# Optimization experiments

Measured on AMD Instinct MI355X. Metric: run time of the kernel, lower is better.

Reference implementation:

```python
import jax, jax.numpy as jnp
import numpy as np

B, S, DIM, NH = 2, 2048, 1024, 8
DH = DIM // NH
GATE_SOFT_CAP = 15.0
BACKEND_EPS = 5e-05
NORM_EPS = 1e-06


def setup_inputs() -> dict:
    key = jax.random.key(0)
    kq, kk, kv, kw = jax.random.split(key, 4)
    q = jax.random.normal(kq, (B, S, DIM), dtype=jnp.float32)
    k = jax.random.normal(kk, (B, S, DIM), dtype=jnp.float32)
    v = jax.random.normal(kv, (B, S, DIM), dtype=jnp.float32)
    # ifgate: Linear(3*dim, 2*num_heads). Init weight is zeros in the module;
    # use small random weights so the gate path is non-trivial.
    ifgate_w = 0.02 * jax.random.normal(kw, (2 * NH, 3 * DIM), dtype=jnp.float32)
    # bias per reset_parameters: i_bias = -10, f_bias = linspace(3, 6, NH)
    ifgate_b = jnp.concatenate([
        jnp.full((NH,), -10.0, dtype=jnp.float32),
        jnp.linspace(3.0, 6.0, NH, dtype=jnp.float32),
    ])
    # residual-weight RMSNorm gain: effective gain = 1 + outnorm_w (init zeros)
    outnorm_w = jnp.zeros((DIM,), dtype=jnp.float32)
    return {"q": q, "k": k, "v": v, "ifgate_w": ifgate_w,
            "ifgate_b": ifgate_b, "outnorm_w": outnorm_w}


def _mlstm_parallel(q, k, v, i_pre, f_pre):
    # q,k,v: (B,NH,S,DH); i_pre,f_pre: (B,NH,S). Native stabilized parallel mLSTM.
    log_fg = jax.nn.log_sigmoid(f_pre)                       # (B,NH,S)
    lf_cs = jnp.cumsum(log_fg, axis=-1)                      # (B,NH,S)
    lf = jnp.concatenate([jnp.zeros_like(lf_cs[..., :1]), lf_cs], axis=-1)  # (B,NH,S+1)
    # log_D[t, s] = sum_{j=s+1}^{t} log_fg[j] + i_pre[s]  for s <= t, else -inf
    log_d = lf[..., 1:, None] - lf[..., None, 1:] + i_pre[..., None, :]     # (B,NH,S,S)
    t_idx = jnp.arange(q.shape[2])
    mask = t_idx[:, None] >= t_idx[None, :]
    log_d = jnp.where(mask, log_d, -jnp.inf)
    m = jnp.max(log_d, axis=-1, keepdims=True)               # (B,NH,S,1)
    d_mat = jnp.exp(log_d - m)                               # stabilized decays
    scores = jnp.einsum("bhtd,bhsd->bhts", q, k) * (1.0 / np.sqrt(DH))
    s_mat = scores * d_mat                                   # (B,NH,S,S)
    denom = jnp.maximum(jnp.abs(jnp.sum(s_mat, axis=-1, keepdims=True)),
                        jnp.exp(-m)) + BACKEND_EPS
    return jnp.einsum("bhts,bhsd->bhtd", s_mat, v) / denom   # (B,NH,S,DH)


def reference(q, k, v, ifgate_w, ifgate_b, outnorm_w):
    b, s, dim = q.shape
    # gate preactivations from concatenated q,k,v with tanh soft cap
    gate_in = jnp.concatenate([q, k, v], axis=-1)            # (B,S,3*DIM)
    pre = gate_in @ ifgate_w.T + ifgate_b                    # (B,S,2*NH)
    pre = GATE_SOFT_CAP * jnp.tanh(pre / GATE_SOFT_CAP)
    i_pre = pre[..., :NH].transpose(0, 2, 1)                 # (B,NH,S)
    f_pre = pre[..., NH:].transpose(0, 2, 1)                 # (B,NH,S)
    # split heads
    qh = q.reshape(b, s, NH, DH).transpose(0, 2, 1, 3)
    kh = k.reshape(b, s, NH, DH).transpose(0, 2, 1, 3)
    vh = v.reshape(b, s, NH, DH).transpose(0, 2, 1, 3)
    h = _mlstm_parallel(qh, kh, vh, i_pre, f_pre)            # (B,NH,S,DH)
    # multi-head RMSNorm with residual gain (bias is unused in the module's forward)
    rrms = jax.lax.rsqrt(jnp.mean(h * h, axis=-1, keepdims=True) + NORM_EPS)
    gain = (1.0 + outnorm_w).reshape(1, NH, 1, DH)
    h = h * rrms * gain
    return h.transpose(0, 2, 1, 3).reshape(b, s, dim)
```

## Files before the change

### kernel.cpp

```cpp
#include <hip/hip_runtime.h>
#include <math.h>

#define BB 2
#define SS 2048
#define DIMM 1024
#define NHH 8
#define DHH 128

constexpr float GATE_CAP = 15.0f;
constexpr float B_EPS = 5e-5f;
constexpr float N_EPS = 1e-6f;
constexpr float K_IS = 0.08838834764831845f;

typedef _Float16 f16x8 __attribute__((ext_vector_type(8)));
typedef __fp16  h16x2 __attribute__((ext_vector_type(2)));
typedef float f32x4 __attribute__((ext_vector_type(4)));

union U8 { f16x8 v; h16x2 h[4]; unsigned int u[4]; };

__device__ inline unsigned short f2bf(float x) {
    unsigned u = __builtin_bit_cast(unsigned, x);
    unsigned r = (u + 0x7fff + ((u >> 16) & 1)) >> 16;
    return (unsigned short)r;
}
__device__ inline float bf2f(unsigned short s) {
    unsigned u = ((unsigned)s) << 16;
    return __builtin_bit_cast(float, u);
}

#define GLD_LDS16(gsrc, ldst)                                                   \
    __builtin_amdgcn_global_load_lds(                                           \
        (const __attribute__((address_space(1))) unsigned int*)(gsrc),          \
        (__attribute__((address_space(3))) unsigned int*)(ldst), 16, 0, 0)

__global__ __launch_bounds__(256) void gate_kernel(
    const float* __restrict__ q, const float* __restrict__ k, const float* __restrict__ v,
    const float* __restrict__ gw, const float* __restrict__ gb,
    float* __restrict__ i_pre, float* __restrict__ lfcs)
{
    __shared__ __align__(16) float xs[2][8][1024];

    const int tid = threadIdx.x;
    const int lane = tid & 63;
    const int wv = tid >> 6;
    const int bs0 = blockIdx.x * 8;

    const float* srcs[3] = {q, k, v};

    auto stage = [&](int buf, int i) {
        const char* src = (const char*)(srcs[i] + (size_t)bs0 * DIMM);
        #pragma unroll
        for (int j = 0; j < 8; ++j) {
            GLD_LDS16(src + j * 4096 + wv * 1024 + lane * 16,
                      (char*)&xs[buf][j][0] + wv * 1024 + lane * 16);
        }
    };

    float acc[8][4];
    #pragma unroll
    for (int r = 0; r < 8; ++r)
        #pragma unroll
        for (int o = 0; o < 4; ++o) acc[r][o] = 0.f;

    stage(0, 0);

    for (int i = 0; i < 3; ++i) {
        const int cur = i & 1;
        if (i < 2) {
            stage(cur ^ 1, i + 1);
            asm volatile("s_waitcnt vmcnt(8)" ::: "memory");
        } else {
            asm volatile("s_waitcnt vmcnt(0)" ::: "memory");
        }
        __builtin_amdgcn_s_barrier();
        __builtin_amdgcn_sched_barrier(0);

        const float* gwi = gw + (wv * 4) * 3 * DIMM + i * DIMM;
        #pragma unroll
        for (int step = 0; step < 4; ++step) {
            float4 w4[4];
            #pragma unroll
            for (int o = 0; o < 4; ++o)
                w4[o] = *(const float4*)&gwi[o * 3 * DIMM + step * 256 + lane * 4];
            #pragma unroll
            for (int r = 0; r < 8; ++r) {
                const float4 xv = *(const float4*)&xs[cur][r][step * 256 + lane * 4];
                #pragma unroll
                for (int o = 0; o < 4; ++o)
                    acc[r][o] += xv.x * w4[o].x + xv.y * w4[o].y
                               + xv.z * w4[o].z + xv.w * w4[o].w;
            }
        }
        __builtin_amdgcn_s_barrier();
    }

    #pragma unroll
    for (int r = 0; r < 8; ++r)
        #pragma unroll
        for (int o = 0; o < 4; ++o) {
            acc[r][o] += __shfl_xor(acc[r][o], 16);
            acc[r][o] += __shfl_xor(acc[r][o], 32);
        }

    float* scr = &xs[0][0][0];
    const int l16 = lane & 15;
    if (l16 == lane) {
        #pragma unroll
        for (int r = 0; r < 8; ++r) {
            float4 st = {acc[r][0], acc[r][1], acc[r][2], acc[r][3]};
            *(float4*)&scr[wv * 576 + l16 * 36 + r * 4] = st;
        }
    }
    __syncthreads();

    if (tid < 128) {
        const int row = tid & 7, o = tid >> 3;
        const float* base = &scr[(o >> 2) * 576 + row * 4 + (o & 3)];
        float s = 0.f;
        #pragma unroll
        for (int j = 0; j < 16; ++j) s += base[j * 36];
        float p = s + gb[o];
        p = GATE_CAP * tanhf(p / GATE_CAP);
        const int bs = bs0 + row;
        const int b = bs >> 11, s2 = bs & 2047;
        if (o < NHH) {
            i_pre[((size_t)b * NHH + o) * SS + s2] = p;
        } else {
            const int h = o - NHH;
            const float ls = (p >= 0.f) ? -log1pf(expf(-p)) : p - log1pf(expf(p));
            lfcs[((size_t)b * NHH + h) * SS + s2] = ls;
        }
    }
}

__global__ __launch_bounds__(256) void prep_kv(
    const float* __restrict__ k, const float* __restrict__ v,
    unsigned short* __restrict__ k16, unsigned short* __restrict__ v16)
{
    const int id = blockIdx.x;
    const int bh = id & 15;
    const int st = id >> 4;
    const int b = bh >> 3, h = bh & 7;
    const int tid = threadIdx.x;

    {
        const float* kp = k + ((size_t)b * SS + st * 64) * DIMM + h * DHH;
        char* kb_ = (char*)k16 + ((size_t)bh * SS + st * 64) * 256;
        #pragma unroll
        for (int j = 0; j < 8; ++j) {
            const int item = j * 256 + tid;
            const int s = item >> 5, dq = item & 31;
            float4 kx = *(const float4*)&kp[(size_t)s * DIMM + dq * 4];
            h16x2 p0 = __builtin_amdgcn_cvt_pkrtz(kx.x, kx.y);
            h16x2 p1 = __builtin_amdgcn_cvt_pkrtz(kx.z, kx.w);
            uint2 wd;
            wd.x = __builtin_bit_cast(unsigned int, p0);
            wd.y = __builtin_bit_cast(unsigned int, p1);
            *(uint2*)(kb_ + s * 256 + ((dq * 8) ^ ((s & 7) << 4))) = wd;
        }
    }

    {
        const int d2 = (tid & 63) * 2;
        const int kb = (tid >> 6) & 1;
        const int gq = tid >> 7;
        const float* vp = v + ((size_t)b * SS + st * 64 + kb * 32) * DIMM + h * DHH + d2;
        char* base = (char*)v16 + ((size_t)bh * 32 + st) * 16384;
        #pragma unroll
        for (int gg = 0; gg < 2; ++gg) {
            const int g = gq * 2 + gg;
            float2 e[8];
            #pragma unroll
            for (int j = 0; j < 8; ++j) {
                const int s = 16 * (j >> 2) + 4 * g + (j & 3);
                e[j] = *(const float2*)&vp[(size_t)s * DIMM];
            }
            U8 u0, u1;
            u0.h[0] = __builtin_amdgcn_cvt_pkrtz(e[0].x, e[1].x);
            u0.h[1] = __builtin_amdgcn_cvt_pkrtz(e[2].x, e[3].x);
            u0.h[2] = __builtin_amdgcn_cvt_pkrtz(e[4].x, e[5].x);
            u0.h[3] = __builtin_amdgcn_cvt_pkrtz(e[6].x, e[7].x);
            u1.h[0] = __builtin_amdgcn_cvt_pkrtz(e[0].y, e[1].y);
            u1.h[1] = __builtin_amdgcn_cvt_pkrtz(e[2].y, e[3].y);
            u1.h[2] = __builtin_amdgcn_cvt_pkrtz(e[4].y, e[5].y);
            u1.h[3] = __builtin_amdgcn_cvt_pkrtz(e[6].y, e[7].y);
            const int p0 = kb * 64 + g * 16;
            *(f16x8*)(base + d2 * 128       + (p0 ^ ((d2 & 7) << 4)))       = u0.v;
            *(f16x8*)(base + (d2 + 1) * 128 + (p0 ^ (((d2 + 1) & 7) << 4))) = u1.v;
        }
    }
}

__global__ __launch_bounds__(256) void scan_kernel(
    const float* __restrict__ i_pre,
    float* __restrict__ lfcs, float* __restrict__ mstab, float* __restrict__ aa)
{
    const int bh = blockIdx.x;
    const int tid = threadIdx.x;
    const int lane = tid & 63, wv = tid >> 6;
    const size_t base = (size_t)bh * SS + tid * 8;

    float x[8];
    {
        float4 a0 = *(const float4*)&lfcs[base];
        float4 a1 = *(const float4*)&lfcs[base + 4];
        x[0] = a0.x; x[1] = a0.y; x[2] = a0.z; x[3] = a0.w;
        x[4] = a1.x; x[5] = a1.y; x[6] = a1.z; x[7] = a1.w;
    }
    #pragma unroll
    for (int i = 1; i < 8; ++i) x[i] += x[i - 1];

    const float tot = x[7];
    float inc = tot;
    #pragma unroll
    for (int off = 1; off < 64; off <<= 1) {
        float n = __shfl_up(inc, off);
        if (lane >= off) inc += n;
    }
    const float exc = inc - tot;

    __shared__ float wt[4], wm[4];
    if (lane == 63) wt[wv] = inc;
    __syncthreads();
    float wpre = 0.f;
    for (int w = 0; w < 4; ++w) if (w < wv) wpre += wt[w];
    const float off0 = exc + wpre;
    #pragma unroll
    for (int i = 0; i < 8; ++i) x[i] += off0;
    {
        float4 s0 = {x[0], x[1], x[2], x[3]}, s1 = {x[4], x[5], x[6], x[7]};
        *(float4*)&lfcs[base] = s0;
        *(float4*)&lfcs[base + 4] = s1;
    }

    float g[8];
    {
        float4 i0 = *(const float4*)&i_pre[base];
        float4 i1 = *(const float4*)&i_pre[base + 4];
        g[0] = i0.x - x[0]; g[1] = i0.y - x[1]; g[2] = i0.z - x[2]; g[3] = i0.w - x[3];
        g[4] = i1.x - x[4]; g[5] = i1.y - x[5]; g[6] = i1.z - x[6]; g[7] = i1.w - x[7];
        float4 s0 = {g[0], g[1], g[2], g[3]}, s1 = {g[4], g[5], g[6], g[7]};
        *(float4*)&aa[base] = s0;
        *(float4*)&aa[base + 4] = s1;
    }
    float mg[8];
    mg[0] = g[0];
    #pragma unroll
    for (int i = 1; i < 8; ++i) mg[i] = fmaxf(mg[i - 1], g[i]);

    float minc = mg[7];
    #pragma unroll
    for (int off = 1; off < 64; off <<= 1) {
        float n = __shfl_up(minc, off);
        if (lane >= off) minc = fmaxf(minc, n);
    }
    float mexc = __shfl_up(minc, 1);
    if (lane == 0) mexc = -1e30f;
    if (lane == 63) wm[wv] = minc;
    __syncthreads();
    float wmpre = -1e30f;
    for (int w = 0; w < 4; ++w) if (w < wv) wmpre = fmaxf(wmpre, wm[w]);
    const float pm = fmaxf(mexc, wmpre);
    float4 s0, s1;
    s0.x = x[0] + fmaxf(pm, mg[0]); s0.y = x[1] + fmaxf(pm, mg[1]);
    s0.z = x[2] + fmaxf(pm, mg[2]); s0.w = x[3] + fmaxf(pm, mg[3]);
    s1.x = x[4] + fmaxf(pm, mg[4]); s1.y = x[5] + fmaxf(pm, mg[5]);
    s1.z = x[6] + fmaxf(pm, mg[6]); s1.w = x[7] + fmaxf(pm, mg[7]);
    *(float4*)&mstab[base] = s0;
    *(float4*)&mstab[base + 4] = s1;
}

__global__ __launch_bounds__(256, 2) void mlstm_splitk(
    const float* __restrict__ q,
    const unsigned short* __restrict__ k16, const unsigned short* __restrict__ v16,
    const float* __restrict__ lfcs, const float* __restrict__ aa,
    unsigned short* __restrict__ pnum, float* __restrict__ pden)
{
    __shared__ __align__(16) unsigned short kbuf[2][8192];
    __shared__ __align__(16) unsigned short vbuf[2][8192];

    const int tid = threadIdx.x;
    const int lane = tid & 63;
    const int wv = tid >> 6;
    const int g = lane >> 4;
    const int l16 = lane & 15;

    const int id = blockIdx.x;
    int bh, qq, chunk;
    if (id < 256) {
        bh = id & 15;
        const int j = id >> 4;
        if (j < 7)       { qq = 5 + j;               chunk = 0; }
        else if (j == 7) { qq = 11;                  chunk = 1; }
        else             { qq = 12 + ((j - 8) >> 1); chunk = (j - 8) & 1; }
    } else {
        const int e = id - 256;
        bh = e & 15;
        const int j = e >> 4;
        if (j < 5)       { qq = j;             chunk = 0; }
        else if (j < 10) { qq = 6 + (j - 5);   chunk = 1; }
        else             { qq = 12 + (j - 10); chunk = 2; }
    }
    const int b = bh >> 3, h = bh & 7;
    const int tw0 = qq * 128 + 32 * wv;

    const size_t bhS = (size_t)bh * SS;
    const float* qp = q + (size_t)b * SS * DIMM + h * DHH;
    const char* kg = (const char*)k16 + (size_t)bh * 524288;
    const char* vg = (const char*)v16 + (size_t)bh * 524288;

    f16x8 qf[2][4];
    float cdec[2];
    #pragma unroll
    for (int nt = 0; nt < 2; ++nt) {
        const int t = tw0 + 16 * nt + l16;
        cdec[nt] = lfcs[bhS + t];
        const float* qrow = qp + (size_t)t * DIMM;
        #pragma unroll
        for (int kb = 0; kb < 4; ++kb) {
            float4 x0 = *(const float4*)&qrow[kb * 32 + g * 8];
            float4 x1 = *(const float4*)&qrow[kb * 32 + g * 8 + 4];
            U8 uu;
            uu.h[0] = __builtin_amdgcn_cvt_pkrtz(x0.x, x0.y);
            uu.h[1] = __builtin_amdgcn_cvt_pkrtz(x0.z, x0.w);
            uu.h[2] = __builtin_amdgcn_cvt_pkrtz(x1.x, x1.y);
            uu.h[3] = __builtin_amdgcn_cvt_pkrtz(x1.z, x1.w);
            qf[nt][kb] = uu.v;
        }
    }

    f32x4 oacc[2][8];
    #pragma unroll
    for (int nt = 0; nt < 2; ++nt)
        #pragma unroll
        for (int mt = 0; mt < 8; ++mt)
            oacc[nt][mt] = (f32x4){0.f, 0.f, 0.f, 0.f};
    float dpart[2] = {0.f, 0.f};

    const int st0 = chunk * 12;
    const int st1m = 2 * qq + 1;
    const int st1 = (st0 + 11 < st1m) ? (st0 + 11) : st1m;

    auto stage = [&](int bi, int st) {
        const char* ksrc = kg + (size_t)st * 16384;
        const char* vsrc = vg + (size_t)st * 16384;
        #pragma unroll
        for (int j = 0; j < 4; ++j) {
            const int off = (j * 4 + wv) * 1024;
            GLD_LDS16(ksrc + off + lane * 16, (char*)&kbuf[bi][0] + off);
            GLD_LDS16(vsrc + off + lane * 16, (char*)&vbuf[bi][0] + off);
        }
    };

    stage(0, st0);

    for (int st = st0; st <= st1; ++st) {
        const int cur = (st - st0) & 1;
        if (st < st1) {
            stage(cur ^ 1, st + 1);
            asm volatile("s_waitcnt vmcnt(8)" ::: "memory");
        } else {
            asm volatile("s_waitcnt vmcnt(0)" ::: "memory");
        }
        __builtin_amdgcn_s_barrier();
        __builtin_amdgcn_sched_barrier(0);

        const int s0 = st * 64;
        const float* ap = aa + bhS + s0;
        f32x4 av[4];
        av[0] = *(const f32x4*)&ap[g * 4];
        av[1] = *(const f32x4*)&ap[16 + g * 4];
        av[2] = *(const f32x4*)&ap[32 + g * 4];
        av[3] = *(const f32x4*)&ap[48 + g * 4];

        f32x4 stacc[2][4];
        #pragma unroll
        for (int nt = 0; nt < 2; ++nt)
            #pragma unroll
            for (int ct = 0; ct < 4; ++ct)
                stacc[nt][ct] = (f32x4){0.f, 0.f, 0.f, 0.f};
        #pragma unroll
        for (int ct = 0; ct < 4; ++ct) {
            const int row = ct * 16 + l16;
            #pragma unroll
            for (int kb = 0; kb < 4; ++kb) {
                f16x8 kf = *(const f16x8*)((const char*)&kbuf[cur][0] +
                            ((row * 256 + kb * 64 + g * 16) ^ ((row & 7) << 4)));
                stacc[0][ct] = __builtin_amdgcn_mfma_f32_16x16x32_f16(kf, qf[0][kb], stacc[0][ct], 0, 0, 0);
                stacc[1][ct] = __builtin_amdgcn_mfma_f32_16x16x32_f16(kf, qf[1][kb], stacc[1][ct], 0, 0, 0);
            }
        }

        const bool diag = (st >= 2 * qq);
        #pragma unroll
        for (int nt = 0; nt < 2; ++nt) {
            float dsum = 0.f;
            const int t_idx = tw0 + nt * 16 + l16;
            #pragma unroll
            for (int ct = 0; ct < 4; ++ct) {
                #pragma unroll
                for (int i = 0; i < 4; ++i) {
                    const float e = K_IS * __expf(cdec[nt] + av[ct][i]);
                    float val = stacc[nt][ct][i] * e;
                    if (diag && (s0 + ct * 16 + g * 4 + i > t_idx)) val = 0.f;
                    dsum += val;
                    stacc[nt][ct][i] = val;
                }
            }
            dpart[nt] += dsum;
        }

        f16x8 pf[2][2];
        #pragma unroll
        for (int nt = 0; nt < 2; ++nt) {
            #pragma unroll
            for (int kb = 0; kb < 2; ++kb) {
                U8 uu;
                uu.h[0] = __builtin_amdgcn_cvt_pkrtz(stacc[nt][2 * kb][0],     stacc[nt][2 * kb][1]);
                uu.h[1] = __builtin_amdgcn_cvt_pkrtz(stacc[nt][2 * kb][2],     stacc[nt][2 * kb][3]);
                uu.h[2] = __builtin_amdgcn_cvt_pkrtz(stacc[nt][2 * kb + 1][0], stacc[nt][2 * kb + 1][1]);
                uu.h[3] = __builtin_amdgcn_cvt_pkrtz(stacc[nt][2 * kb + 1][2], stacc[nt][2 * kb + 1][3]);
                pf[nt][kb] = uu.v;
            }
        }

        #pragma unroll
        for (int mt = 0; mt < 8; ++mt) {
            const int dI = mt * 16 + l16;
            #pragma unroll
            for (int kb = 0; kb < 2; ++kb) {
                f16x8 vf = *(const f16x8*)((const char*)&vbuf[cur][0] +
                            dI * 128 + ((kb * 64 + g * 16) ^ ((dI & 7) << 4)));
                oacc[0][mt] = __builtin_amdgcn_mfma_f32_16x16x32_f16(vf, pf[0][kb], oacc[0][mt], 0, 0, 0);
                oacc[1][mt] = __builtin_amdgcn_mfma_f32_16x16x32_f16(vf, pf[1][kb], oacc[1][mt], 0, 0, 0);
            }
        }
        __builtin_amdgcn_sched_barrier(0);
        __builtin_amdgcn_s_barrier();
    }

    const int uoff = (qq < 6) ? qq : ((qq < 12) ? (6 + 2 * (qq - 6)) : (18 + 3 * (qq - 12)));
    const size_t cidx = (size_t)bh * 30 + uoff + chunk;
    #pragma unroll
    for (int nt = 0; nt < 2; ++nt) {
        float den = dpart[nt];
        den += __shfl_xor(den, 16);
        den += __shfl_xor(den, 32);
        const int row = wv * 32 + nt * 16 + l16;
        if (g == 0) pden[cidx * 128 + row] = den;
        #pragma unroll
        for (int mt = 0; mt < 8; ++mt) {
            ushort4 pk;
            pk.x = f2bf(oacc[nt][mt][0]);
            pk.y = f2bf(oacc[nt][mt][1]);
            pk.z = f2bf(oacc[nt][mt][2]);
            pk.w = f2bf(oacc[nt][mt][3]);
            *(ushort4*)&pnum[((cidx * 64 + wv * 16 + nt * 8 + mt) << 8) + lane * 4] = pk;
        }
    }
}

__global__ __launch_bounds__(256) void reduce_kernel(
    const unsigned short* __restrict__ pnum, const float* __restrict__ pden,
    const float* __restrict__ mstab, const float* __restrict__ onw,
    float* __restrict__ out)
{
    const int id = blockIdx.x;
    const int bh = id & 15;
    const int qq = id >> 4;
    const int b = bh >> 3, h = bh & 7;
    const int tid = threadIdx.x;
    const int lane = tid & 63;
    const int wv = tid >> 6;
    const int g = lane >> 4;
    const int l16 = lane & 15;

    const int nch = (qq < 6) ? 1 : ((qq < 12) ? 2 : 3);
    const int uoff = (qq < 6) ? qq : ((qq < 12) ? (6 + 2 * (qq - 6)) : (18 + 3 * (qq - 12)));
    const size_t cbase = (size_t)bh * 30 + uoff;

    f32x4 acc[2][8];
    #pragma unroll
    for (int nt = 0; nt < 2; ++nt)
        #pragma unroll
        for (int mt = 0; mt < 8; ++mt)
            acc[nt][mt] = (f32x4){0.f, 0.f, 0.f, 0.f};
    float den[2] = {0.f, 0.f};

    for (int c = 0; c < nch; ++c) {
        const size_t fb = (cbase + c) * 64 + wv * 16;
        #pragma unroll
        for (int nt = 0; nt < 2; ++nt) {
            #pragma unroll
            for (int mt = 0; mt < 8; ++mt) {
                ushort4 t4 = *(const ushort4*)&pnum[((fb + nt * 8 + mt) << 8) + lane * 4];
                acc[nt][mt][0] += bf2f(t4.x);
                acc[nt][mt][1] += bf2f(t4.y);
                acc[nt][mt][2] += bf2f(t4.z);
                acc[nt][mt][3] += bf2f(t4.w);
            }
            den[nt] += pden[(cbase + c) * 128 + wv * 32 + nt * 16 + l16];
        }
    }

    #pragma unroll
    for (int nt = 0; nt < 2; ++nt) {
        const int t = qq * 128 + wv * 32 + nt * 16 + l16;
        const float m = mstab[(size_t)bh * SS + t];
        const float em = __expf(-m);
        const float dt = den[nt] * em;
        const float denf = fmaxf(fabsf(dt), em) + B_EPS;
        const float inv = em / denf;
        float ssq = 0.f;
        #pragma unroll
        for (int mt = 0; mt < 8; ++mt) {
            #pragma unroll
            for (int i = 0; i < 4; ++i) {
                acc[nt][mt][i] *= inv;
                ssq += acc[nt][mt][i] * acc[nt][mt][i];
            }
        }
        ssq += __shfl_xor(ssq, 16);
        ssq += __shfl_xor(ssq, 32);
        const float rms = rsqrtf(ssq * (1.0f / DHH) + N_EPS);

        float* orow = out + ((size_t)b * SS + t) * DIMM + h * DHH;
        #pragma unroll
        for (int mt = 0; mt < 8; ++mt) {
            float4 gn = *(const float4*)&onw[h * DHH + mt * 16 + g * 4];
            float4 o4;
            o4.x = acc[nt][mt][0] * rms * (1.f + gn.x);
            o4.y = acc[nt][mt][1] * rms * (1.f + gn.y);
            o4.z = acc[nt][mt][2] * rms * (1.f + gn.z);
            o4.w = acc[nt][mt][3] * rms * (1.f + gn.w);
            *(float4*)&orow[mt * 16 + g * 4] = o4;
        }
    }
}

extern "C" void kernel_launch(void* const* d_in, const int* in_sizes, int n_in,
                              void* d_out, int out_size, void* d_ws, size_t ws_size,
                              hipStream_t stream) {
    const float* q   = (const float*)d_in[0];
    const float* k   = (const float*)d_in[1];
    const float* v   = (const float*)d_in[2];
    const float* gw  = (const float*)d_in[3];
    const float* gb  = (const float*)d_in[4];
    const float* onw = (const float*)d_in[5];
    float* out = (float*)d_out;

    float* ws    = (float*)d_ws;
    float* i_pre = ws;
    float* lfcs  = ws + 32768;
    float* mm    = ws + 65536;
    float* aa    = ws + 98304;
    float* pden  = ws + 131072;
    unsigned short* pnum = (unsigned short*)((char*)d_ws + 1048576);
    unsigned short* k16  = (unsigned short*)((char*)d_ws + 16777216);
    unsigned short* v16  = (unsigned short*)((char*)d_ws + 25165824);

    hipLaunchKernelGGL(gate_kernel, dim3(BB * SS / 8), dim3(256), 0, stream,
                       q, k, v, gw, gb, i_pre, lfcs);
    hipLaunchKernelGGL(prep_kv, dim3(16 * 32), dim3(256), 0, stream, k, v, k16, v16);
    hipLaunchKernelGGL(scan_kernel, dim3(BB * NHH), dim3(256), 0, stream, i_pre, lfcs, mm, aa);
    hipLaunchKernelGGL(mlstm_splitk, dim3(480), dim3(256), 0, stream,
                       q, k16, v16, lfcs, aa, pnum, pden);
    hipLaunchKernelGGL(reduce_kernel, dim3(16 * 16), dim3(256), 0, stream,
                       pnum, pden, mm, onw, out);
}
```

Measured before the change: 84.07 us.

## Restructure mLSTM into per-wave tasks, fuse K conversion into gate and V prep into scan

The K fp16 conversion moves into the gate kernel, which reuses the k rows it already stages in shared memory. The V conversion merges with the scan into one launch, which removes a kernel. The main kernel now gives each wave an independent 32-row query task over up to four key tiles. It reads K and V fragments straight from global memory in a pre-swizzled MFMA layout instead of double-buffering them through LDS, so there are no block barriers. The decay exponentials are split into a per-column factor (precomputed in the scan) and a per-row factor, which cuts the exp work in the inner loop, but partial sums grow and the reduce kernel has to walk a task index.

```diff
diff --git a/kernel.cpp b/kernel.cpp
--- a/kernel.cpp
+++ b/kernel.cpp
@@ -10,7 +10,8 @@
 constexpr float GATE_CAP = 15.0f;
 constexpr float B_EPS = 5e-5f;
 constexpr float N_EPS = 1e-6f;
-constexpr float K_IS = 0.08838834764831845f;
+constexpr float LOG2E = 1.4426950408889634f;
+constexpr float LN_KIS = -2.4260151319598084f;
 
 typedef _Float16 f16x8 __attribute__((ext_vector_type(8)));
 typedef __fp16  h16x2 __attribute__((ext_vector_type(2)));
@@ -27,6 +28,7 @@
     unsigned u = ((unsigned)s) << 16;
     return __builtin_bit_cast(float, u);
 }
+__device__ inline int nck_of(int tg) { return ((tg >> 1) + 4) >> 2; }
 
 #define GLD_LDS16(gsrc, ldst)                                                   \
     __builtin_amdgcn_global_load_lds(                                           \
@@ -36,7 +38,8 @@
 __global__ __launch_bounds__(256) void gate_kernel(
     const float* __restrict__ q, const float* __restrict__ k, const float* __restrict__ v,
     const float* __restrict__ gw, const float* __restrict__ gb,
-    float* __restrict__ i_pre, float* __restrict__ lfcs)
+    float* __restrict__ i_pre, float* __restrict__ lfcs,
+    unsigned short* __restrict__ k16)
 {
     __shared__ __align__(16) float xs[2][8][1024];
 
@@ -66,6 +69,14 @@
 
     for (int i = 0; i < 3; ++i) {
         const int cur = i & 1;
+        const float* gwi = gw + (wv * 4) * 3 * DIMM + i * DIMM;
+        float4 w4[4][4];
+        #pragma unroll
+        for (int step = 0; step < 4; ++step)
+            #pragma unroll
+            for (int o = 0; o < 4; ++o)
+                w4[step][o] = *(const float4*)&gwi[o * 3 * DIMM + step * 256 + lane * 4];
+
         if (i < 2) {
             stage(cur ^ 1, i + 1);
             asm volatile("s_waitcnt vmcnt(8)" ::: "memory");
@@ -75,23 +86,44 @@
         __builtin_amdgcn_s_barrier();
         __builtin_amdgcn_sched_barrier(0);
 
-        const float* gwi = gw + (wv * 4) * 3 * DIMM + i * DIMM;
         #pragma unroll
         for (int step = 0; step < 4; ++step) {
-            float4 w4[4];
-            #pragma unroll
-            for (int o = 0; o < 4; ++o)
-                w4[o] = *(const float4*)&gwi[o * 3 * DIMM + step * 256 + lane * 4];
             #pragma unroll
             for (int r = 0; r < 8; ++r) {
                 const float4 xv = *(const float4*)&xs[cur][r][step * 256 + lane * 4];
                 #pragma unroll
                 for (int o = 0; o < 4; ++o)
-                    acc[r][o] += xv.x * w4[o].x + xv.y * w4[o].y
-                               + xv.z * w4[o].z + xv.w * w4[o].w;
+                    acc[r][o] += xv.x * w4[step][o].x + xv.y * w4[step][o].y
+                               + xv.z * w4[step][o].z + xv.w * w4[step][o].w;
             }
         }
         __builtin_amdgcn_s_barrier();
+    }
+
+    #pragma unroll
+    for (int it = 0; it < 8; ++it) {
+        const int item = it * 256 + tid;
+        const int r = item >> 8;
+        const int dq = item & 255;
+        const int hh = dq >> 6;
+        (void)hh;
+        const int head = dq >> 5;
+        const int dqh = dq & 31;
+        const int kb = dqh >> 3;
+        const int g = (dqh >> 1) & 3;
+        const int half = dqh & 1;
+        float4 kx = *(const float4*)&xs[1][r][dq * 4];
+        h16x2 p0 = __builtin_amdgcn_cvt_pkrtz(kx.x, kx.y);
+        h16x2 p1 = __builtin_amdgcn_cvt_pkrtz(kx.z, kx.w);
+        uint2 wd;
+        wd.x = __builtin_bit_cast(unsigned int, p0);
+        wd.y = __builtin_bit_cast(unsigned int, p1);
+        const int bs = bs0 + r;
+        const int b = bs >> 11, s2 = bs & 2047;
+        const size_t bh = (size_t)b * NHH + head;
+        const int st = s2 >> 6, ct = (s2 >> 4) & 3, l16k = s2 & 15;
+        *(uint2*)((char*)k16 + bh * 524288 + (size_t)st * 16384 +
+                  (ct * 4 + kb) * 1024 + (g * 16 + l16k) * 16 + half * 8) = wd;
     }
 
     #pragma unroll
@@ -107,8 +139,8 @@
     if (l16 == lane) {
         #pragma unroll
         for (int r = 0; r < 8; ++r) {
-            float4 st = {acc[r][0], acc[r][1], acc[r][2], acc[r][3]};
-            *(float4*)&scr[wv * 576 + l16 * 36 + r * 4] = st;
+            float4 st4 = {acc[r][0], acc[r][1], acc[r][2], acc[r][3]};
+            *(float4*)&scr[wv * 576 + l16 * 36 + r * 4] = st4;
         }
     }
     __syncthreads();
@@ -133,39 +165,25 @@
     }
 }
 
-__global__ __launch_bounds__(256) void prep_kv(
-    const float* __restrict__ k, const float* __restrict__ v,
-    unsigned short* __restrict__ k16, unsigned short* __restrict__ v16)
+__global__ __launch_bounds__(256) void vscan_kernel(
+    const float* __restrict__ v, unsigned short* __restrict__ v16,
+    const float* __restrict__ i_pre,
+    float* __restrict__ lfcs, float* __restrict__ mstab, float* __restrict__ aa,
+    float* __restrict__ lf0)
 {
     const int id = blockIdx.x;
-    const int bh = id & 15;
-    const int st = id >> 4;
-    const int b = bh >> 3, h = bh & 7;
     const int tid = threadIdx.x;
-
-    {
-        const float* kp = k + ((size_t)b * SS + st * 64) * DIMM + h * DHH;
-        char* kb_ = (char*)k16 + ((size_t)bh * SS + st * 64) * 256;
-        #pragma unroll
-        for (int j = 0; j < 8; ++j) {
-            const int item = j * 256 + tid;
-            const int s = item >> 5, dq = item & 31;
-            float4 kx = *(const float4*)&kp[(size_t)s * DIMM + dq * 4];
-            h16x2 p0 = __builtin_amdgcn_cvt_pkrtz(kx.x, kx.y);
-            h16x2 p1 = __builtin_amdgcn_cvt_pkrtz(kx.z, kx.w);
-            uint2 wd;
-            wd.x = __builtin_bit_cast(unsigned int, p0);
-            wd.y = __builtin_bit_cast(unsigned int, p1);
-            *(uint2*)(kb_ + s * 256 + ((dq * 8) ^ ((s & 7) << 4))) = wd;
-        }
-    }
-
-    {
+    __shared__ float wt[4], wm[4];
+
+    if (id < 512) {
+        const int bh = id & 15;
+        const int st = id >> 4;
+        const int b = bh >> 3, h = bh & 7;
         const int d2 = (tid & 63) * 2;
         const int kb = (tid >> 6) & 1;
         const int gq = tid >> 7;
         const float* vp = v + ((size_t)b * SS + st * 64 + kb * 32) * DIMM + h * DHH + d2;
-        char* base = (char*)v16 + ((size_t)bh * 32 + st) * 16384;
+        char* base = (char*)v16 + (size_t)bh * 524288 + (size_t)st * 16384 + kb * 8192;
         #pragma unroll
         for (int gg = 0; gg < 2; ++gg) {
             const int g = gq * 2 + gg;
@@ -184,19 +202,13 @@
             u1.h[1] = __builtin_amdgcn_cvt_pkrtz(e[2].y, e[3].y);
             u1.h[2] = __builtin_amdgcn_cvt_pkrtz(e[4].y, e[5].y);
             u1.h[3] = __builtin_amdgcn_cvt_pkrtz(e[6].y, e[7].y);
-            const int p0 = kb * 64 + g * 16;
-            *(f16x8*)(base + d2 * 128       + (p0 ^ ((d2 & 7) << 4)))       = u0.v;
-            *(f16x8*)(base + (d2 + 1) * 128 + (p0 ^ (((d2 + 1) & 7) << 4))) = u1.v;
-        }
-    }
-}
-
-__global__ __launch_bounds__(256) void scan_kernel(
-    const float* __restrict__ i_pre,
-    float* __restrict__ lfcs, float* __restrict__ mstab, float* __restrict__ aa)
-{
-    const int bh = blockIdx.x;
-    const int tid = threadIdx.x;
+            *(f16x8*)(base + (d2 >> 4) * 1024 + (g * 16 + (d2 & 15)) * 16)             = u0.v;
+            *(f16x8*)(base + ((d2 + 1) >> 4) * 1024 + (g * 16 + ((d2 + 1) & 15)) * 16) = u1.v;
+        }
+        return;
+    }
+
+    const int bh = id - 512;
     const int lane = tid & 63, wv = tid >> 6;
     const size_t base = (size_t)bh * SS + tid * 8;
 
@@ -219,7 +231,6 @@
     }
     const float exc = inc - tot;
 
-    __shared__ float wt[4], wm[4];
     if (lane == 63) wt[wv] = inc;
     __syncthreads();
     float wpre = 0.f;
@@ -232,6 +243,9 @@
         *(float4*)&lfcs[base] = s0;
         *(float4*)&lfcs[base + 4] = s1;
     }
+
+    const float p0t = __shfl(off0, lane & 56);
+    if ((tid & 7) == 0) lf0[bh * 32 + (tid >> 3)] = off0;
 
     float g[8];
     {
@@ -239,7 +253,15 @@
         float4 i1 = *(const float4*)&i_pre[base + 4];
         g[0] = i0.x - x[0]; g[1] = i0.y - x[1]; g[2] = i0.z - x[2]; g[3] = i0.w - x[3];
         g[4] = i1.x - x[4]; g[5] = i1.y - x[5]; g[6] = i1.z - x[6]; g[7] = i1.w - x[7];
-        float4 s0 = {g[0], g[1], g[2], g[3]}, s1 = {g[4], g[5], g[6], g[7]};
+        float4 s0, s1;
+        s0.x = __builtin_amdgcn_exp2f((g[0] + p0t) * LOG2E);
+        s0.y = __builtin_amdgcn_exp2f((g[1] + p0t) * LOG2E);
+        s0.z = __builtin_amdgcn_exp2f((g[2] + p0t) * LOG2E);
+        s0.w = __builtin_amdgcn_exp2f((g[3] + p0t) * LOG2E);
+        s1.x = __builtin_amdgcn_exp2f((g[4] + p0t) * LOG2E);
+        s1.y = __builtin_amdgcn_exp2f((g[5] + p0t) * LOG2E);
+        s1.z = __builtin_amdgcn_exp2f((g[6] + p0t) * LOG2E);
+        s1.w = __builtin_amdgcn_exp2f((g[7] + p0t) * LOG2E);
         *(float4*)&aa[base] = s0;
         *(float4*)&aa[base + 4] = s1;
     }
@@ -270,51 +292,44 @@
     *(float4*)&mstab[base + 4] = s1;
 }
 
-__global__ __launch_bounds__(256, 2) void mlstm_splitk(
+__global__ __launch_bounds__(256, 2) void mlstm_wave(
     const float* __restrict__ q,
     const unsigned short* __restrict__ k16, const unsigned short* __restrict__ v16,
     const float* __restrict__ lfcs, const float* __restrict__ aa,
+    const float* __restrict__ lf0,
     unsigned short* __restrict__ pnum, float* __restrict__ pden)
 {
-    __shared__ __align__(16) unsigned short kbuf[2][8192];
-    __shared__ __align__(16) unsigned short vbuf[2][8192];
-
     const int tid = threadIdx.x;
     const int lane = tid & 63;
     const int wv = tid >> 6;
     const int g = lane >> 4;
     const int l16 = lane & 15;
 
-    const int id = blockIdx.x;
-    int bh, qq, chunk;
-    if (id < 256) {
-        bh = id & 15;
-        const int j = id >> 4;
-        if (j < 7)       { qq = 5 + j;               chunk = 0; }
-        else if (j == 7) { qq = 11;                  chunk = 1; }
-        else             { qq = 12 + ((j - 8) >> 1); chunk = (j - 8) & 1; }
-    } else {
-        const int e = id - 256;
-        bh = e & 15;
-        const int j = e >> 4;
-        if (j < 5)       { qq = j;             chunk = 0; }
-        else if (j < 10) { qq = 6 + (j - 5);   chunk = 1; }
-        else             { qq = 12 + (j - 10); chunk = 2; }
-    }
+    const int task = blockIdx.x + wv * 1152;
+    const int bh = task & 15;
+    int u = task >> 4;
+    int tg = 63;
+    while (true) {
+        const int n = nck_of(tg);
+        if (u < n) break;
+        u -= n;
+        --tg;
+    }
+    const int ck = u;
     const int b = bh >> 3, h = bh & 7;
-    const int tw0 = qq * 128 + 32 * wv;
+    const int t0 = tg * 32;
 
     const size_t bhS = (size_t)bh * SS;
     const float* qp = q + (size_t)b * SS * DIMM + h * DHH;
-    const char* kg = (const char*)k16 + (size_t)bh * 524288;
-    const char* vg = (const char*)v16 + (size_t)bh * 524288;
+    const char* kgf = (const char*)k16 + (size_t)bh * 524288;
+    const char* vgf = (const char*)v16 + (size_t)bh * 524288;
 
     f16x8 qf[2][4];
-    float cdec[2];
+    float cdec2[2];
     #pragma unroll
     for (int nt = 0; nt < 2; ++nt) {
-        const int t = tw0 + 16 * nt + l16;
-        cdec[nt] = lfcs[bhS + t];
+        const int t = t0 + nt * 16 + l16;
+        cdec2[nt] = (lfcs[bhS + t] + LN_KIS) * LOG2E;
         const float* qrow = qp + (size_t)t * DIMM;
         #pragma unroll
         for (int kb = 0; kb < 4; ++kb) {
@@ -337,34 +352,11 @@
             oacc[nt][mt] = (f32x4){0.f, 0.f, 0.f, 0.f};
     float dpart[2] = {0.f, 0.f};
 
-    const int st0 = chunk * 12;
-    const int st1m = 2 * qq + 1;
-    const int st1 = (st0 + 11 < st1m) ? (st0 + 11) : st1m;
-
-    auto stage = [&](int bi, int st) {
-        const char* ksrc = kg + (size_t)st * 16384;
-        const char* vsrc = vg + (size_t)st * 16384;
-        #pragma unroll
-        for (int j = 0; j < 4; ++j) {
-            const int off = (j * 4 + wv) * 1024;
-            GLD_LDS16(ksrc + off + lane * 16, (char*)&kbuf[bi][0] + off);
-            GLD_LDS16(vsrc + off + lane * 16, (char*)&vbuf[bi][0] + off);
-        }
-    };
-
-    stage(0, st0);
+    const int stmax = tg >> 1;
+    const int st0 = ck * 4;
+    const int st1 = (st0 + 3 < stmax) ? (st0 + 3) : stmax;
 
     for (int st = st0; st <= st1; ++st) {
-        const int cur = (st - st0) & 1;
-        if (st < st1) {
-            stage(cur ^ 1, st + 1);
-            asm volatile("s_waitcnt vmcnt(8)" ::: "memory");
-        } else {
-            asm volatile("s_waitcnt vmcnt(0)" ::: "memory");
-        }
-        __builtin_amdgcn_s_barrier();
-        __builtin_amdgcn_sched_barrier(0);
-
         const int s0 = st * 64;
         const float* ap = aa + bhS + s0;
         f32x4 av[4];
@@ -372,6 +364,14 @@
         av[1] = *(const f32x4*)&ap[16 + g * 4];
         av[2] = *(const f32x4*)&ap[32 + g * 4];
         av[3] = *(const f32x4*)&ap[48 + g * 4];
+        const float lf0l2 = lf0[bh * 32 + st] * LOG2E;
+        float rowf[2];
+        rowf[0] = __builtin_amdgcn_exp2f(cdec2[0] - lf0l2);
+        rowf[1] = __builtin_amdgcn_exp2f(cdec2[1] - lf0l2);
+
+        const char* kt = kgf + (size_t)st * 16384;
+        const char* vt = vgf + (size_t)st * 16384;
+        const bool diag = (st == stmax);
 
         f32x4 stacc[2][4];
         #pragma unroll
@@ -379,40 +379,33 @@
             #pragma unroll
             for (int ct = 0; ct < 4; ++ct)
                 stacc[nt][ct] = (f32x4){0.f, 0.f, 0.f, 0.f};
+
         #pragma unroll
         for (int ct = 0; ct < 4; ++ct) {
-            const int row = ct * 16 + l16;
             #pragma unroll
             for (int kb = 0; kb < 4; ++kb) {
-                f16x8 kf = *(const f16x8*)((const char*)&kbuf[cur][0] +
-                            ((row * 256 + kb * 64 + g * 16) ^ ((row & 7) << 4)));
+                f16x8 kf = *(const f16x8*)(kt + (ct * 4 + kb) * 1024 + lane * 16);
                 stacc[0][ct] = __builtin_amdgcn_mfma_f32_16x16x32_f16(kf, qf[0][kb], stacc[0][ct], 0, 0, 0);
                 stacc[1][ct] = __builtin_amdgcn_mfma_f32_16x16x32_f16(kf, qf[1][kb], stacc[1][ct], 0, 0, 0);
             }
         }
 
-        const bool diag = (st >= 2 * qq);
+        f16x8 pf[2][2];
         #pragma unroll
         for (int nt = 0; nt < 2; ++nt) {
             float dsum = 0.f;
-            const int t_idx = tw0 + nt * 16 + l16;
+            const int t_idx = t0 + nt * 16 + l16;
             #pragma unroll
             for (int ct = 0; ct < 4; ++ct) {
                 #pragma unroll
                 for (int i = 0; i < 4; ++i) {
-                    const float e = K_IS * __expf(cdec[nt] + av[ct][i]);
-                    float val = stacc[nt][ct][i] * e;
+                    float val = stacc[nt][ct][i] * av[ct][i] * rowf[nt];
                     if (diag && (s0 + ct * 16 + g * 4 + i > t_idx)) val = 0.f;
                     dsum += val;
                     stacc[nt][ct][i] = val;
                 }
             }
             dpart[nt] += dsum;
-        }
-
-        f16x8 pf[2][2];
-        #pragma unroll
-        for (int nt = 0; nt < 2; ++nt) {
             #pragma unroll
             for (int kb = 0; kb < 2; ++kb) {
                 U8 uu;
@@ -426,28 +419,22 @@
 
         #pragma unroll
         for (int mt = 0; mt < 8; ++mt) {
-            const int dI = mt * 16 + l16;
             #pragma unroll
             for (int kb = 0; kb < 2; ++kb) {
-                f16x8 vf = *(const f16x8*)((const char*)&vbuf[cur][0] +
-                            dI * 128 + ((kb * 64 + g * 16) ^ ((dI & 7) << 4)));
+                f16x8 vf = *(const f16x8*)(vt + kb * 8192 + mt * 1024 + lane * 16);
                 oacc[0][mt] = __builtin_amdgcn_mfma_f32_16x16x32_f16(vf, pf[0][kb], oacc[0][mt], 0, 0, 0);
                 oacc[1][mt] = __builtin_amdgcn_mfma_f32_16x16x32_f16(vf, pf[1][kb], oacc[1][mt], 0, 0, 0);
             }
         }
-        __builtin_amdgcn_sched_barrier(0);
-        __builtin_amdgcn_s_barrier();
-    }
-
-    const int uoff = (qq < 6) ? qq : ((qq < 12) ? (6 + 2 * (qq - 6)) : (18 + 3 * (qq - 12)));
-    const size_t cidx = (size_t)bh * 30 + uoff + chunk;
+    }
+
+    const size_t cidx = (size_t)task;
     #pragma unroll
     for (int nt = 0; nt < 2; ++nt) {
         float den = dpart[nt];
         den += __shfl_xor(den, 16);
         den += __shfl_xor(den, 32);
-        const int row = wv * 32 + nt * 16 + l16;
-        if (g == 0) pden[cidx * 128 + row] = den;
+        if (g == 0) pden[cidx * 32 + nt * 16 + l16] = den;
         #pragma unroll
         for (int mt = 0; mt < 8; ++mt) {
             ushort4 pk;
@@ -455,7 +442,7 @@
             pk.y = f2bf(oacc[nt][mt][1]);
             pk.z = f2bf(oacc[nt][mt][2]);
             pk.w = f2bf(oacc[nt][mt][3]);
-            *(ushort4*)&pnum[((cidx * 64 + wv * 16 + nt * 8 + mt) << 8) + lane * 4] = pk;
+            *(ushort4*)&pnum[(cidx * 16 + nt * 8 + mt) * 256 + lane * 4] = pk;
         }
     }
 }
@@ -465,19 +452,19 @@
     const float* __restrict__ mstab, const float* __restrict__ onw,
     float* __restrict__ out)
 {
-    const int id = blockIdx.x;
-    const int bh = id & 15;
-    const int qq = id >> 4;
-    const int b = bh >> 3, h = bh & 7;
     const int tid = threadIdx.x;
     const int lane = tid & 63;
-    const int wv = tid >> 6;
+    const int wvi = tid >> 6;
+    const int id = blockIdx.x * 4 + wvi;
+    const int bh = id & 15;
+    const int tg = id >> 4;
+    const int b = bh >> 3, h = bh & 7;
     const int g = lane >> 4;
     const int l16 = lane & 15;
 
-    const int nch = (qq < 6) ? 1 : ((qq < 12) ? 2 : 3);
-    const int uoff = (qq < 6) ? qq : ((qq < 12) ? (6 + 2 * (qq - 6)) : (18 + 3 * (qq - 12)));
-    const size_t cbase = (size_t)bh * 30 + uoff;
+    int ub = 0;
+    for (int t2 = 63; t2 > tg; --t2) ub += nck_of(t2);
+    const int nch = nck_of(tg);
 
     f32x4 acc[2][8];
     #pragma unroll
@@ -488,24 +475,24 @@
     float den[2] = {0.f, 0.f};
 
     for (int c = 0; c < nch; ++c) {
-        const size_t fb = (cbase + c) * 64 + wv * 16;
+        const size_t cidx = (size_t)(ub + c) * 16 + bh;
         #pragma unroll
         for (int nt = 0; nt < 2; ++nt) {
             #pragma unroll
             for (int mt = 0; mt < 8; ++mt) {
-                ushort4 t4 = *(const ushort4*)&pnum[((fb + nt * 8 + mt) << 8) + lane * 4];
+                ushort4 t4 = *(const ushort4*)&pnum[(cidx * 16 + nt * 8 + mt) * 256 + lane * 4];
                 acc[nt][mt][0] += bf2f(t4.x);
                 acc[nt][mt][1] += bf2f(t4.y);
                 acc[nt][mt][2] += bf2f(t4.z);
                 acc[nt][mt][3] += bf2f(t4.w);
             }
-            den[nt] += pden[(cbase + c) * 128 + wv * 32 + nt * 16 + l16];
+            den[nt] += pden[cidx * 32 + nt * 16 + l16];
         }
     }
 
     #pragma unroll
     for (int nt = 0; nt < 2; ++nt) {
-        const int t = qq * 128 + wv * 32 + nt * 16 + l16;
+        const int t = tg * 32 + nt * 16 + l16;
         const float m = mstab[(size_t)bh * SS + t];
         const float em = __expf(-m);
         const float dt = den[nt] * em;
@@ -554,17 +541,18 @@
     float* lfcs  = ws + 32768;
     float* mm    = ws + 65536;
     float* aa    = ws + 98304;
-    float* pden  = ws + 131072;
-    unsigned short* pnum = (unsigned short*)((char*)d_ws + 1048576);
-    unsigned short* k16  = (unsigned short*)((char*)d_ws + 16777216);
-    unsigned short* v16  = (unsigned short*)((char*)d_ws + 25165824);
+    float* lf0   = ws + 131072;
+    float* pden  = ws + 133120;
+    unsigned short* pnum = (unsigned short*)((char*)d_ws + 2097152);
+    unsigned short* k16  = (unsigned short*)((char*)d_ws + 41943040);
+    unsigned short* v16  = (unsigned short*)((char*)d_ws + 50331648);
 
     hipLaunchKernelGGL(gate_kernel, dim3(BB * SS / 8), dim3(256), 0, stream,
-                       q, k, v, gw, gb, i_pre, lfcs);
-    hipLaunchKernelGGL(prep_kv, dim3(16 * 32), dim3(256), 0, stream, k, v, k16, v16);
-    hipLaunchKernelGGL(scan_kernel, dim3(BB * NHH), dim3(256), 0, stream, i_pre, lfcs, mm, aa);
-    hipLaunchKernelGGL(mlstm_splitk, dim3(480), dim3(256), 0, stream,
-                       q, k16, v16, lfcs, aa, pnum, pden);
-    hipLaunchKernelGGL(reduce_kernel, dim3(16 * 16), dim3(256), 0, stream,
+                       q, k, v, gw, gb, i_pre, lfcs, k16);
+    hipLaunchKernelGGL(vscan_kernel, dim3(528), dim3(256), 0, stream,
+                       v, v16, i_pre, lfcs, mm, aa, lf0);
+    hipLaunchKernelGGL(mlstm_wave, dim3(1152), dim3(256), 0, stream,
+                       q, k16, v16, lfcs, aa, lf0, pnum, pden);
+    hipLaunchKernelGGL(reduce_kernel, dim3(256), dim3(256), 0, stream,
                        pnum, pden, mm, onw, out);
 }
```

Result: faster. 80.22 us (-4.6%).
